# Performance work log

Measured on AMD Instinct MI355X. Metric: run time of the kernel, lower is better.

Reference implementation:

```python
import jax, jax.numpy as jnp
import numpy as np

N = 50000
HEADS1, HIM = 8, 16
NEG_SLOPE = 0.2


def gat_conv(x, src, dst, W, a_src, a_dst, bias, heads, out_dim, concat):
    n = x.shape[0]
    h = (x @ W).reshape(n, heads, out_dim)                      # [N,H,D]
    al_src = jnp.einsum('nhd,hd->nh', h, a_src)                  # [N,H]
    al_dst = jnp.einsum('nhd,hd->nh', h, a_dst)                  # [N,H]
    e = jax.nn.leaky_relu(al_src[src] + al_dst[dst], NEG_SLOPE)  # [E,H]
    # segment softmax over incoming edges of each destination node
    e_max = jax.ops.segment_max(e, dst, num_segments=n)
    e_max = jnp.where(jnp.isfinite(e_max), e_max, 0.0)
    ex = jnp.exp(e - e_max[dst])
    denom = jax.ops.segment_sum(ex, dst, num_segments=n)
    denom = jnp.where(denom == 0.0, 1.0, denom)
    alpha = ex / denom[dst]                                      # [E,H]
    msg = h[src] * alpha[:, :, None]                             # [E,H,D]
    out = jax.ops.segment_sum(msg, dst, num_segments=n)          # [N,H,D]
    out = out.reshape(n, heads * out_dim) if concat else out.mean(axis=1)
    return out + bias


def setup_inputs() -> dict:
    key = jax.random.key(0)
    ks = jax.random.split(key, 12)
    num_feature, out_feature, him = 128, 121, HIM
    E = 800000
    x = jax.random.normal(ks[0], (N, num_feature), dtype=jnp.float32)
    edge_index = jax.random.randint(ks[1], (2, E), 0, N, dtype=jnp.int64)
    s = 0.1
    W1 = jax.random.normal(ks[2], (num_feature, HEADS1 * him), dtype=jnp.float32) * s
    a_src1 = jax.random.normal(ks[3], (HEADS1, him), dtype=jnp.float32) * s
    a_dst1 = jax.random.normal(ks[4], (HEADS1, him), dtype=jnp.float32) * s
    b1 = jnp.zeros((HEADS1 * him,), dtype=jnp.float32)
    W2 = jax.random.normal(ks[5], (HEADS1 * him, out_feature), dtype=jnp.float32) * s
    a_src2 = jax.random.normal(ks[6], (1, out_feature), dtype=jnp.float32) * s
    a_dst2 = jax.random.normal(ks[7], (1, out_feature), dtype=jnp.float32) * s
    b2 = jnp.zeros((out_feature,), dtype=jnp.float32)
    return {"x": x, "edge_index": edge_index, "W1": W1, "a_src1": a_src1,
            "a_dst1": a_dst1, "b1": b1, "W2": W2, "a_src2": a_src2,
            "a_dst2": a_dst2, "b2": b2}


def reference(x, edge_index, W1, a_src1, a_dst1, b1, W2, a_src2, a_dst2, b2):
    n = x.shape[0]
    loops = jnp.arange(n, dtype=edge_index.dtype)
    src = jnp.concatenate([edge_index[0], loops])  # add self-loops (PyG default)
    dst = jnp.concatenate([edge_index[1], loops])
    h = gat_conv(x, src, dst, W1, a_src1, a_dst1, b1, HEADS1, HIM, True)
    h = jax.nn.relu(h)
    out = gat_conv(h, src, dst, W2, a_src2, a_dst2, b2, 1, W2.shape[1], True)
    return out
```

## Files before the change

### kernel.cpp

```cpp
#include <hip/hip_runtime.h>
#include <hip/hip_fp16.h>

#define NEG_SLOPE 0.2f

typedef __fp16 half8v __attribute__((ext_vector_type(8)));
typedef float f32x4 __attribute__((ext_vector_type(4)));

__device__ __forceinline__ float lrelu(float x) {
    return fmaxf(x, 0.0f) + NEG_SLOPE * fminf(x, 0.0f);
}

__device__ __forceinline__ unsigned fkey(float f) {
    unsigned u = __float_as_uint(f);
    return (u & 0x80000000u) ? ~u : (u | 0x80000000u);
}
__device__ __forceinline__ float funkey(unsigned k) {
    return __uint_as_float((k & 0x80000000u) ? (k & 0x7fffffffu) : ~k);
}


__global__ void pack_kernel(const int* __restrict__ src, const int* __restrict__ dst,
                            unsigned* __restrict__ kv, int E) {
    int e = blockIdx.x * 256 + threadIdx.x;
    if (e < E) kv[e] = ((unsigned)dst[e] << 16) | (unsigned)src[e];
}


__global__ __launch_bounds__(256) void scan_reduce(const int* __restrict__ cnt,
                                                   int* __restrict__ bsum, int n) {
    __shared__ int sm[256];
    int base = blockIdx.x * 1024 + threadIdx.x * 4;
    int s = 0;
#pragma unroll
    for (int j = 0; j < 4; ++j) {
        int i = base + j;
        if (i < n) s += cnt[i];
    }
    sm[threadIdx.x] = s;
    __syncthreads();
#pragma unroll
    for (int off = 128; off >= 1; off >>= 1) {
        if (threadIdx.x < off) sm[threadIdx.x] += sm[threadIdx.x + off];
        __syncthreads();
    }
    if (threadIdx.x == 0) bsum[blockIdx.x] = sm[0];
}

__global__ __launch_bounds__(64) void scan_bsum(int* __restrict__ bsum, int nb) {
    int v = (threadIdx.x < (unsigned)nb) ? bsum[threadIdx.x] : 0;
    int x = v;
#pragma unroll
    for (int off = 1; off < 64; off <<= 1) {
        int y = __shfl_up(x, off);
        if ((int)threadIdx.x >= off) x += y;
    }
    if (threadIdx.x < (unsigned)nb) bsum[threadIdx.x] = x - v;
}

__global__ __launch_bounds__(256) void scan_write(const int* __restrict__ cnt,
                                                  const int* __restrict__ bsum,
                                                  int* __restrict__ rp, int n) {
    __shared__ int sm[256];
    int base = blockIdx.x * 1024 + threadIdx.x * 4;
    int v[4];
    int s = 0;
#pragma unroll
    for (int j = 0; j < 4; ++j) {
        int i = base + j;
        v[j] = (i < n) ? cnt[i] : 0;
        s += v[j];
    }
    sm[threadIdx.x] = s;
    __syncthreads();
#pragma unroll
    for (int off = 1; off < 256; off <<= 1) {
        int y = (threadIdx.x >= off) ? sm[threadIdx.x - off] : 0;
        __syncthreads();
        sm[threadIdx.x] += y;
        __syncthreads();
    }
    int run = sm[threadIdx.x] - s + bsum[blockIdx.x];
#pragma unroll
    for (int j = 0; j < 4; ++j) {
        int i = base + j;
        if (i < n) {
            rp[i] = run;
            run += v[j];
            if (i == n - 1) rp[n] = run;
        }
    }
}


template <int SH>
__global__ __launch_bounds__(256) void rhist_kernel(const unsigned* __restrict__ kv,
                                                    int* __restrict__ h, int E, int nblk) {
    __shared__ int lh[256];
    lh[threadIdx.x] = 0;
    __syncthreads();
    int base = blockIdx.x * 4096;
#pragma unroll
    for (int j = 0; j < 16; ++j) {
        int i = base + j * 256 + threadIdx.x;
        if (i < E) atomicAdd(&lh[(kv[i] >> SH) & 255], 1);
    }
    __syncthreads();
    h[threadIdx.x * nblk + blockIdx.x] = lh[threadIdx.x];
}


template <int SH>
__global__ __launch_bounds__(256) void rscat_kernel(const unsigned* __restrict__ in,
                                                    unsigned* __restrict__ outv,
                                                    const int* __restrict__ scanned,
                                                    int E, int nblk) {
    __shared__ unsigned items[4096];
    __shared__ unsigned sorted[4096];
    __shared__ int lh[256], lstart[256], rbase[256];
    __shared__ int wcnt[4][256];

    int tid = threadIdx.x, blk = blockIdx.x;
    int base = blk * 4096;
    int k = min(4096, E - base);
    lh[tid] = 0;
    rbase[tid] = 0;
#pragma unroll
    for (int j = 0; j < 16; ++j) {
        int idx = j * 256 + tid;
        items[idx] = (base + idx < E) ? in[base + idx] : 0u;
    }
    __syncthreads();
#pragma unroll
    for (int j = 0; j < 16; ++j) {
        int idx = j * 256 + tid;
        if (idx < k) atomicAdd(&lh[(items[idx] >> SH) & 255], 1);
    }
    __syncthreads();
    int sv = lh[tid];
    lstart[tid] = sv;
    __syncthreads();
    for (int off = 1; off < 256; off <<= 1) {
        int y = (tid >= off) ? lstart[tid - off] : 0;
        __syncthreads();
        lstart[tid] += y;
        __syncthreads();
    }
    int excl = lstart[tid] - sv;
    __syncthreads();
    lstart[tid] = excl;
    __syncthreads();

    int lane = tid & 63, wave = tid >> 6;
    for (int it = 0; it < 16; ++it) {
        int idx = it * 256 + tid;
        unsigned v = items[idx];
        int d = (v >> SH) & 255;
        bool valid = idx < k;
        unsigned long long vm = __ballot(valid);
        unsigned long long m = vm;
#pragma unroll
        for (int b = 0; b < 8; ++b) {
            unsigned long long bb = __ballot((d >> b) & 1);
            m &= ((d >> b) & 1) ? bb : ~bb;
        }
        int lanerank = __popcll(m & ((1ull << lane) - 1ull));
        int wtot = __popcll(m);
        wcnt[0][tid] = 0; wcnt[1][tid] = 0; wcnt[2][tid] = 0; wcnt[3][tid] = 0;
        __syncthreads();
        if (valid && lanerank == 0) wcnt[wave][d] = wtot;
        __syncthreads();
        if (valid) {
            int cw = 0;
            for (int w = 0; w < wave; ++w) cw += wcnt[w][d];
            sorted[lstart[d] + rbase[d] + cw + lanerank] = v;
        }
        __syncthreads();
        rbase[tid] += wcnt[0][tid] + wcnt[1][tid] + wcnt[2][tid] + wcnt[3][tid];
        __syncthreads();
    }
#pragma unroll
    for (int j = 0; j < 16; ++j) {
        int i = j * 256 + tid;
        if (i < k) {
            unsigned v = sorted[i];
            int d = (v >> SH) & 255;
            outv[scanned[d * nblk + blk] + (i - lstart[d])] = v;
        }
    }
}


__global__ void rp_kernel(const unsigned* __restrict__ kv, int* __restrict__ rp,
                          int E, int N) {
    int i = blockIdx.x * 256 + threadIdx.x;
    if (i >= E) return;
    int cur = (int)(kv[i] >> 16);
    int prev = (i == 0) ? -1 : (int)(kv[i - 1] >> 16);
    for (int t = prev + 1; t <= cur; ++t) rp[t] = i;
    if (i == E - 1)
        for (int t = cur + 1; t <= N; ++t) rp[t] = E;
}


template <int H>
__global__ __launch_bounds__(256) void gmax_kernel(const float* __restrict__ a,
                                                   unsigned* __restrict__ gm, int total) {
    __shared__ unsigned sm[256];
    unsigned loc = 0;
    int stride = 256 * gridDim.x;
    for (int i = blockIdx.x * 256 + threadIdx.x; i < total; i += stride)
        loc = max(loc, fkey(a[i]));
    sm[threadIdx.x] = loc;
    __syncthreads();
    for (int off = 128; off >= H; off >>= 1) {
        if (threadIdx.x < off) sm[threadIdx.x] = max(sm[threadIdx.x], sm[threadIdx.x + off]);
        __syncthreads();
    }
    if (threadIdx.x < H) atomicMax(&gm[threadIdx.x], sm[threadIdx.x]);
}


__global__ __launch_bounds__(256) void cvt_half_kernel(const float* __restrict__ in,
                                                       __half* __restrict__ out, int total8) {
    int i = blockIdx.x * 256 + threadIdx.x;
    if (i >= total8) return;
    const float4* ip = (const float4*)in + (size_t)i * 2;
    float4 a = ip[0], b = ip[1];
    union { float4 f4; __half2 h[4]; } u;
    u.h[0] = __floats2half2_rn(a.x, a.y);
    u.h[1] = __floats2half2_rn(a.z, a.w);
    u.h[2] = __floats2half2_rn(b.x, b.y);
    u.h[3] = __floats2half2_rn(b.z, b.w);
    *((float4*)out + i) = u.f4;
}


template <int NC>
__global__ __launch_bounds__(256) void gemm_mfma(const __half* __restrict__ A,
                                                 const float* __restrict__ B,
                                                 __half* __restrict__ C, int M) {
    __shared__ __half Bt[128][136];

    {
        int t = threadIdx.x;
        int c = t & 127;
        int kq = t >> 7;
#pragma unroll
        for (int ch = 0; ch < 8; ++ch) {
            int k0 = kq * 64 + ch * 8;
            half8v hv;
#pragma unroll
            for (int j = 0; j < 8; ++j) {
                float v = (c < NC) ? B[(size_t)(k0 + j) * NC + c] : 0.0f;
                hv[j] = (__fp16)v;
            }
            *(half8v*)&Bt[c][k0] = hv;
        }
    }
    __syncthreads();

    const int wid = threadIdx.x >> 6;
    const int lane = threadIdx.x & 63;
    const int li = lane & 15;
    const int lg = lane >> 4;

    int row = blockIdx.x * 64 + wid * 16 + li;
    int rowc = min(row, M - 1);
    const half8v* Ap = (const half8v*)(A + (size_t)rowc * 128);

    half8v a[4];
#pragma unroll
    for (int ks = 0; ks < 4; ++ks) a[ks] = Ap[ks * 4 + lg];

    f32x4 acc[8];
#pragma unroll
    for (int ct = 0; ct < 8; ++ct) acc[ct] = (f32x4)0.0f;

#pragma unroll
    for (int ks = 0; ks < 4; ++ks) {
#pragma unroll
        for (int ct = 0; ct < 8; ++ct) {
            half8v b = *(const half8v*)&Bt[ct * 16 + li][ks * 32 + 8 * lg];
            acc[ct] = __builtin_amdgcn_mfma_f32_16x16x32_f16(a[ks], b, acc[ct], 0, 0, 0);
        }
    }

    int orow = blockIdx.x * 64 + wid * 16 + 4 * lg;
#pragma unroll
    for (int ct = 0; ct < 8; ++ct) {
#pragma unroll
        for (int r = 0; r < 4; ++r) {
            int rr = orow + r;
            if (rr < M) C[(size_t)rr * 128 + ct * 16 + li] = __float2half(acc[ct][r]);
        }
    }
}


__global__ void al1_kernel(const __half* __restrict__ h1h, const float* __restrict__ as,
                           const float* __restrict__ ad, float* __restrict__ alS,
                           float* __restrict__ alD, int N) {
    int g = blockIdx.x * 256 + threadIdx.x;
    if (g >= N * 8) return;
    int r = g >> 3, h = g & 7;
    const __half2* hp = (const __half2*)(h1h + (size_t)r * 128 + h * 16);
    const float* sp = as + h * 16;
    const float* dp = ad + h * 16;
    float s = 0.f, d = 0.f;
#pragma unroll
    for (int q = 0; q < 8; ++q) {
        float2 v = __half22float2(hp[q]);
        s = fmaf(v.x, sp[2 * q], s);
        d = fmaf(v.x, dp[2 * q], d);
        s = fmaf(v.y, sp[2 * q + 1], s);
        d = fmaf(v.y, dp[2 * q + 1], d);
    }
    alS[g] = s;
    alD[g] = d;
}

__global__ __launch_bounds__(256) void al2_kernel(const __half* __restrict__ h3h,
                                                  const float* __restrict__ as,
                                                  const float* __restrict__ ad,
                                                  float* __restrict__ alS,
                                                  float* __restrict__ alD, int N, int NC) {
    int lane = threadIdx.x & 63;
    int r = blockIdx.x * 4 + (threadIdx.x >> 6);
    if (r >= N) return;
    float s = 0.f, d = 0.f;
    for (int c = lane; c < NC; c += 64) {
        float v = __half2float(h3h[(size_t)r * 128 + c]);
        s = fmaf(v, as[c], s);
        d = fmaf(v, ad[c], d);
    }
#pragma unroll
    for (int off = 32; off; off >>= 1) {
        s += __shfl_down(s, off);
        d += __shfl_down(d, off);
    }
    if (lane == 0) { alS[r] = s; alD[r] = d; }
}


__global__ __launch_bounds__(256) void agg1_kernel(
    const __half* __restrict__ h1h, const float* __restrict__ alS,
    const float* __restrict__ alD, const float* __restrict__ b1,
    const int* __restrict__ rp, const unsigned* __restrict__ kv,
    const unsigned* __restrict__ gm, __half* __restrict__ h2h, int N) {
    int t = blockIdx.x * 4 + (threadIdx.x >> 6);
    if (t >= N) return;
    int lane = threadIdx.x & 63;
    int h = lane >> 3;

    float adh = alD[t * 8 + h];
    float mh = lrelu(funkey(gm[h]) + adh);
    int e0 = rp[t], e1 = rp[t + 1];

    float ex = __expf(lrelu(alS[t * 8 + h] + adh) - mh);
    float dsum = ex;
    float2 hs = __half22float2(*(const __half2*)(h1h + (size_t)t * 128 + 2 * lane));
    float fx = ex * hs.x, fy = ex * hs.y;

    int e = e0;
    for (; e + 4 <= e1; e += 4) {
        int s0 = (int)(kv[e] & 0xFFFFu), s1 = (int)(kv[e + 1] & 0xFFFFu);
        int s2 = (int)(kv[e + 2] & 0xFFFFu), s3 = (int)(kv[e + 3] & 0xFFFFu);
        float w0 = __expf(lrelu(alS[s0 * 8 + h] + adh) - mh);
        float w1 = __expf(lrelu(alS[s1 * 8 + h] + adh) - mh);
        float w2 = __expf(lrelu(alS[s2 * 8 + h] + adh) - mh);
        float w3 = __expf(lrelu(alS[s3 * 8 + h] + adh) - mh);
        float2 f0 = __half22float2(*(const __half2*)(h1h + (size_t)s0 * 128 + 2 * lane));
        float2 f1 = __half22float2(*(const __half2*)(h1h + (size_t)s1 * 128 + 2 * lane));
        float2 f2 = __half22float2(*(const __half2*)(h1h + (size_t)s2 * 128 + 2 * lane));
        float2 f3 = __half22float2(*(const __half2*)(h1h + (size_t)s3 * 128 + 2 * lane));
        dsum += (w0 + w1) + (w2 + w3);
        fx = fmaf(w0, f0.x, fx); fy = fmaf(w0, f0.y, fy);
        fx = fmaf(w1, f1.x, fx); fy = fmaf(w1, f1.y, fy);
        fx = fmaf(w2, f2.x, fx); fy = fmaf(w2, f2.y, fy);
        fx = fmaf(w3, f3.x, fx); fy = fmaf(w3, f3.y, fy);
    }
    for (; e < e1; ++e) {
        int s0 = (int)(kv[e] & 0xFFFFu);
        float w0 = __expf(lrelu(alS[s0 * 8 + h] + adh) - mh);
        float2 f0 = __half22float2(*(const __half2*)(h1h + (size_t)s0 * 128 + 2 * lane));
        dsum += w0;
        fx = fmaf(w0, f0.x, fx); fy = fmaf(w0, f0.y, fy);
    }
    float inv = 1.0f / dsum;
    float2 bb = *(const float2*)(b1 + 2 * lane);
    float ox = fmaxf(fmaf(fx, inv, bb.x), 0.0f);
    float oy = fmaxf(fmaf(fy, inv, bb.y), 0.0f);
    *(__half2*)(h2h + (size_t)t * 128 + 2 * lane) = __floats2half2_rn(ox, oy);
}


__global__ __launch_bounds__(256) void agg2_kernel(
    const __half* __restrict__ h3h, const float* __restrict__ alS,
    const float* __restrict__ alD, const float* __restrict__ b2,
    const int* __restrict__ rp, const unsigned* __restrict__ kv,
    const unsigned* __restrict__ gm, float* __restrict__ out, int N, int NC) {
    int t = blockIdx.x * 4 + (threadIdx.x >> 6);
    if (t >= N) return;
    int lane = threadIdx.x & 63;

    float adT = alD[t];
    float m = lrelu(funkey(gm[0]) + adT);
    int e0 = rp[t], e1 = rp[t + 1];

    float ex = __expf(lrelu(alS[t] + adT) - m);
    float dsum = ex;
    float2 hs = __half22float2(*(const __half2*)(h3h + (size_t)t * 128 + 2 * lane));
    float fx = ex * hs.x, fy = ex * hs.y;

    int e = e0;
    for (; e + 4 <= e1; e += 4) {
        int s0 = (int)(kv[e] & 0xFFFFu), s1 = (int)(kv[e + 1] & 0xFFFFu);
        int s2 = (int)(kv[e + 2] & 0xFFFFu), s3 = (int)(kv[e + 3] & 0xFFFFu);
        float w0 = __expf(lrelu(alS[s0] + adT) - m);
        float w1 = __expf(lrelu(alS[s1] + adT) - m);
        float w2 = __expf(lrelu(alS[s2] + adT) - m);
        float w3 = __expf(lrelu(alS[s3] + adT) - m);
        float2 f0 = __half22float2(*(const __half2*)(h3h + (size_t)s0 * 128 + 2 * lane));
        float2 f1 = __half22float2(*(const __half2*)(h3h + (size_t)s1 * 128 + 2 * lane));
        float2 f2 = __half22float2(*(const __half2*)(h3h + (size_t)s2 * 128 + 2 * lane));
        float2 f3 = __half22float2(*(const __half2*)(h3h + (size_t)s3 * 128 + 2 * lane));
        dsum += (w0 + w1) + (w2 + w3);
        fx = fmaf(w0, f0.x, fx); fy = fmaf(w0, f0.y, fy);
        fx = fmaf(w1, f1.x, fx); fy = fmaf(w1, f1.y, fy);
        fx = fmaf(w2, f2.x, fx); fy = fmaf(w2, f2.y, fy);
        fx = fmaf(w3, f3.x, fx); fy = fmaf(w3, f3.y, fy);
    }
    for (; e < e1; ++e) {
        int s0 = (int)(kv[e] & 0xFFFFu);
        float w0 = __expf(lrelu(alS[s0] + adT) - m);
        float2 f0 = __half22float2(*(const __half2*)(h3h + (size_t)s0 * 128 + 2 * lane));
        dsum += w0;
        fx = fmaf(w0, f0.x, fx); fy = fmaf(w0, f0.y, fy);
    }
    float inv = 1.0f / dsum;
    int c0 = 2 * lane, c1 = 2 * lane + 1;
    if (c0 < NC) out[(size_t)t * NC + c0] = fmaf(fx, inv, b2[c0]);
    if (c1 < NC) out[(size_t)t * NC + c1] = fmaf(fy, inv, b2[c1]);
}


extern "C" void kernel_launch(void* const* d_in, const int* in_sizes, int n_in,
                              void* d_out, int out_size, void* d_ws, size_t ws_size,
                              hipStream_t stream) {
    const float* x   = (const float*)d_in[0];
    const int*   ei  = (const int*)d_in[1];
    const float* W1  = (const float*)d_in[2];
    const float* aS1 = (const float*)d_in[3];
    const float* aD1 = (const float*)d_in[4];
    const float* b1  = (const float*)d_in[5];
    const float* W2  = (const float*)d_in[6];
    const float* aS2 = (const float*)d_in[7];
    const float* aD2 = (const float*)d_in[8];
    const float* b2  = (const float*)d_in[9];
    float* out = (float*)d_out;

    const int N = in_sizes[0] / 128;
    const int E = in_sizes[1] / 2;
    const int NC2 = 121;

    const int NBLK = (E + 4095) / 4096;
    const int HN = 256 * NBLK;

    size_t off = 0;
    auto alloc = [&](size_t bytes) {
        size_t o = off;
        off = (off + bytes + 255) & ~(size_t)255;
        return o;
    };
    char* ws = (char*)d_ws;
    unsigned* kv0  = (unsigned*)(ws + alloc((size_t)E * 4));
    unsigned* kv1  = (unsigned*)(ws + alloc((size_t)E * 4));
    int*      h    = (int*)(ws + alloc((size_t)(HN + 1) * 4));
    int*      hs   = (int*)(ws + alloc((size_t)(HN + 1) * 4));
    int*      rp   = (int*)(ws + alloc((size_t)(N + 1) * 4));
    int*      bsum = (int*)(ws + alloc(64 * 4));
    float*    alS1 = (float*)(ws + alloc((size_t)N * 8 * 4));
    float*    alD1 = (float*)(ws + alloc((size_t)N * 8 * 4));
    float*    alS2 = (float*)(ws + alloc((size_t)N * 4));
    float*    alD2 = (float*)(ws + alloc((size_t)N * 4));
    unsigned* gm1  = (unsigned*)(ws + alloc(8 * 4));
    unsigned* gm2  = (unsigned*)(ws + alloc(4));
    __half*   xh   = (__half*)(ws + alloc((size_t)N * 128 * 2));
    __half*   h1h  = (__half*)(ws + alloc((size_t)N * 128 * 2));
    __half*   h2h  = (__half*)(ws + alloc((size_t)N * 128 * 2));
    __half*   h3h  = h1h;
    if (ws_size < off) return;

    const int* src = ei;
    const int* dst = ei + E;

    hipMemsetAsync(gm1, 0, 8 * 4, stream);
    hipMemsetAsync(gm2, 0, 4, stream);

    int eb = (E + 255) / 256;
    int snb = (HN + 1023) / 1024;

    pack_kernel<<<eb, 256, 0, stream>>>(src, dst, kv0, E);
    rhist_kernel<16><<<NBLK, 256, 0, stream>>>(kv0, h, E, NBLK);
    scan_reduce<<<snb, 256, 0, stream>>>(h, bsum, HN);
    scan_bsum<<<1, 64, 0, stream>>>(bsum, snb);
    scan_write<<<snb, 256, 0, stream>>>(h, bsum, hs, HN);
    rscat_kernel<16><<<NBLK, 256, 0, stream>>>(kv0, kv1, hs, E, NBLK);
    rhist_kernel<24><<<NBLK, 256, 0, stream>>>(kv1, h, E, NBLK);
    scan_reduce<<<snb, 256, 0, stream>>>(h, bsum, HN);
    scan_bsum<<<1, 64, 0, stream>>>(bsum, snb);
    scan_write<<<snb, 256, 0, stream>>>(h, bsum, hs, HN);
    rscat_kernel<24><<<NBLK, 256, 0, stream>>>(kv1, kv0, hs, E, NBLK);
    rp_kernel<<<eb, 256, 0, stream>>>(kv0, rp, E, N);

    int cvb = (N * 128 / 8 + 255) / 256;
    cvt_half_kernel<<<cvb, 256, 0, stream>>>(x, xh, N * 128 / 8);

    int gmb = (N + 63) / 64;
    int ab = (N + 3) / 4;
    gemm_mfma<128><<<gmb, 256, 0, stream>>>(xh, W1, h1h, N);
    al1_kernel<<<(N * 8 + 255) / 256, 256, 0, stream>>>(h1h, aS1, aD1, alS1, alD1, N);
    gmax_kernel<8><<<128, 256, 0, stream>>>(alS1, gm1, N * 8);
    agg1_kernel<<<ab, 256, 0, stream>>>(h1h, alS1, alD1, b1, rp, kv0, gm1, h2h, N);

    gemm_mfma<121><<<gmb, 256, 0, stream>>>(h2h, W2, h3h, N);
    al2_kernel<<<ab, 256, 0, stream>>>(h3h, aS2, aD2, alS2, alD2, N, NC2);
    gmax_kernel<1><<<128, 256, 0, stream>>>(alS2, gm2, N);
    agg2_kernel<<<ab, 256, 0, stream>>>(h3h, alS2, alD2, b2, rp, kv0, gm2, out, N, NC2);
}
```

Measured before the change: 237.3 us.

## Precompute per-edge attention weights and fuse fp32-to-half conversion into GEMM

Drops the separate x-to-half conversion kernel; the first GEMM now loads fp32 rows and converts them in registers. Per-edge exponentiated attention weights are computed in new edge-parallel kernels (stored as half for layer 1, float for layer 2). The aggregation kernels then read these weights sequentially instead of gathering alS per source and recomputing exp, and each splits the denominator sum into two accumulators. The cost is two extra launches and extra traffic to write and reread the edge-weight arrays, and layer 1 weights lose precision by being stored in half.

```diff
diff --git a/kernel.cpp b/kernel.cpp
--- a/kernel.cpp
+++ b/kernel.cpp
@@ -156,8 +156,7 @@
         unsigned v = items[idx];
         int d = (v >> SH) & 255;
         bool valid = idx < k;
-        unsigned long long vm = __ballot(valid);
-        unsigned long long m = vm;
+        unsigned long long m = __ballot(valid);
 #pragma unroll
         for (int b = 0; b < 8; ++b) {
             unsigned long long bb = __ballot((d >> b) & 1);
@@ -220,23 +219,34 @@
 }
 
 
-__global__ __launch_bounds__(256) void cvt_half_kernel(const float* __restrict__ in,
-                                                       __half* __restrict__ out, int total8) {
-    int i = blockIdx.x * 256 + threadIdx.x;
-    if (i >= total8) return;
-    const float4* ip = (const float4*)in + (size_t)i * 2;
-    float4 a = ip[0], b = ip[1];
-    union { float4 f4; __half2 h[4]; } u;
-    u.h[0] = __floats2half2_rn(a.x, a.y);
-    u.h[1] = __floats2half2_rn(a.z, a.w);
-    u.h[2] = __floats2half2_rn(b.x, b.y);
-    u.h[3] = __floats2half2_rn(b.z, b.w);
-    *((float4*)out + i) = u.f4;
-}
-
-
-template <int NC>
-__global__ __launch_bounds__(256) void gemm_mfma(const __half* __restrict__ A,
+__global__ void w1_kernel(const unsigned* __restrict__ kv, const float* __restrict__ alS,
+                          const float* __restrict__ alD, const unsigned* __restrict__ gm,
+                          __half* __restrict__ w1v, int E8) {
+    int g = blockIdx.x * 256 + threadIdx.x;
+    if (g >= E8) return;
+    int e = g >> 3, h = g & 7;
+    unsigned k = kv[e];
+    int s = (int)(k & 0xFFFFu), t = (int)(k >> 16);
+    float adT = alD[t * 8 + h];
+    float m = lrelu(funkey(gm[h]) + adT);
+    w1v[g] = __float2half(__expf(lrelu(alS[s * 8 + h] + adT) - m));
+}
+
+
+__global__ void w2_kernel(const unsigned* __restrict__ kv, const float* __restrict__ alS,
+                          const float* __restrict__ alD, const unsigned* __restrict__ gm,
+                          float* __restrict__ w2v, int E) {
+    int e = blockIdx.x * 256 + threadIdx.x;
+    if (e >= E) return;
+    unsigned k = kv[e];
+    int s = (int)(k & 0xFFFFu), t = (int)(k >> 16);
+    float adT = alD[t];
+    w2v[e] = __expf(lrelu(alS[s] + adT) - lrelu(funkey(gm[0]) + adT));
+}
+
+
+template <int NC, typename AT>
+__global__ __launch_bounds__(256) void gemm_mfma(const AT* __restrict__ A,
                                                  const float* __restrict__ B,
                                                  __half* __restrict__ C, int M) {
     __shared__ __half Bt[128][136];
@@ -266,11 +276,22 @@
 
     int row = blockIdx.x * 64 + wid * 16 + li;
     int rowc = min(row, M - 1);
-    const half8v* Ap = (const half8v*)(A + (size_t)rowc * 128);
 
     half8v a[4];
 #pragma unroll
-    for (int ks = 0; ks < 4; ++ks) a[ks] = Ap[ks * 4 + lg];
+    for (int ks = 0; ks < 4; ++ks) {
+        int q = ks * 4 + lg;
+        if constexpr (sizeof(AT) == 2) {
+            a[ks] = *((const half8v*)(A + (size_t)rowc * 128) + q);
+        } else {
+            const float4* p = (const float4*)(A + (size_t)rowc * 128) + 2 * q;
+            float4 a0 = p[0], a1 = p[1];
+            half8v hv;
+            hv[0] = (__fp16)a0.x; hv[1] = (__fp16)a0.y; hv[2] = (__fp16)a0.z; hv[3] = (__fp16)a0.w;
+            hv[4] = (__fp16)a1.x; hv[5] = (__fp16)a1.y; hv[6] = (__fp16)a1.z; hv[7] = (__fp16)a1.w;
+            a[ks] = hv;
+        }
+    }
 
     f32x4 acc[8];
 #pragma unroll
@@ -346,7 +367,8 @@
     const __half* __restrict__ h1h, const float* __restrict__ alS,
     const float* __restrict__ alD, const float* __restrict__ b1,
     const int* __restrict__ rp, const unsigned* __restrict__ kv,
-    const unsigned* __restrict__ gm, __half* __restrict__ h2h, int N) {
+    const __half* __restrict__ w1v, const unsigned* __restrict__ gm,
+    __half* __restrict__ h2h, int N) {
     int t = blockIdx.x * 4 + (threadIdx.x >> 6);
     if (t >= N) return;
     int lane = threadIdx.x & 63;
@@ -357,7 +379,7 @@
     int e0 = rp[t], e1 = rp[t + 1];
 
     float ex = __expf(lrelu(alS[t * 8 + h] + adh) - mh);
-    float dsum = ex;
+    float dsum = ex, dsum2 = 0.f;
     float2 hs = __half22float2(*(const __half2*)(h1h + (size_t)t * 128 + 2 * lane));
     float fx = ex * hs.x, fy = ex * hs.y;
 
@@ -365,15 +387,16 @@
     for (; e + 4 <= e1; e += 4) {
         int s0 = (int)(kv[e] & 0xFFFFu), s1 = (int)(kv[e + 1] & 0xFFFFu);
         int s2 = (int)(kv[e + 2] & 0xFFFFu), s3 = (int)(kv[e + 3] & 0xFFFFu);
-        float w0 = __expf(lrelu(alS[s0 * 8 + h] + adh) - mh);
-        float w1 = __expf(lrelu(alS[s1 * 8 + h] + adh) - mh);
-        float w2 = __expf(lrelu(alS[s2 * 8 + h] + adh) - mh);
-        float w3 = __expf(lrelu(alS[s3 * 8 + h] + adh) - mh);
+        float w0 = __half2float(w1v[(size_t)(e + 0) * 8 + h]);
+        float w1 = __half2float(w1v[(size_t)(e + 1) * 8 + h]);
+        float w2 = __half2float(w1v[(size_t)(e + 2) * 8 + h]);
+        float w3 = __half2float(w1v[(size_t)(e + 3) * 8 + h]);
         float2 f0 = __half22float2(*(const __half2*)(h1h + (size_t)s0 * 128 + 2 * lane));
         float2 f1 = __half22float2(*(const __half2*)(h1h + (size_t)s1 * 128 + 2 * lane));
         float2 f2 = __half22float2(*(const __half2*)(h1h + (size_t)s2 * 128 + 2 * lane));
         float2 f3 = __half22float2(*(const __half2*)(h1h + (size_t)s3 * 128 + 2 * lane));
-        dsum += (w0 + w1) + (w2 + w3);
+        dsum += w0 + w1;
+        dsum2 += w2 + w3;
         fx = fmaf(w0, f0.x, fx); fy = fmaf(w0, f0.y, fy);
         fx = fmaf(w1, f1.x, fx); fy = fmaf(w1, f1.y, fy);
         fx = fmaf(w2, f2.x, fx); fy = fmaf(w2, f2.y, fy);
@@ -381,11 +404,12 @@
     }
     for (; e < e1; ++e) {
         int s0 = (int)(kv[e] & 0xFFFFu);
-        float w0 = __expf(lrelu(alS[s0 * 8 + h] + adh) - mh);
+        float w0 = __half2float(w1v[(size_t)e * 8 + h]);
         float2 f0 = __half22float2(*(const __half2*)(h1h + (size_t)s0 * 128 + 2 * lane));
         dsum += w0;
         fx = fmaf(w0, f0.x, fx); fy = fmaf(w0, f0.y, fy);
     }
+    dsum += dsum2;
     float inv = 1.0f / dsum;
     float2 bb = *(const float2*)(b1 + 2 * lane);
     float ox = fmaxf(fmaf(fx, inv, bb.x), 0.0f);
@@ -398,7 +422,8 @@
     const __half* __restrict__ h3h, const float* __restrict__ alS,
     const float* __restrict__ alD, const float* __restrict__ b2,
     const int* __restrict__ rp, const unsigned* __restrict__ kv,
-    const unsigned* __restrict__ gm, float* __restrict__ out, int N, int NC) {
+    const float* __restrict__ w2v, const unsigned* __restrict__ gm,
+    float* __restrict__ out, int N, int NC) {
     int t = blockIdx.x * 4 + (threadIdx.x >> 6);
     if (t >= N) return;
     int lane = threadIdx.x & 63;
@@ -408,7 +433,7 @@
     int e0 = rp[t], e1 = rp[t + 1];
 
     float ex = __expf(lrelu(alS[t] + adT) - m);
-    float dsum = ex;
+    float dsum = ex, dsum2 = 0.f;
     float2 hs = __half22float2(*(const __half2*)(h3h + (size_t)t * 128 + 2 * lane));
     float fx = ex * hs.x, fy = ex * hs.y;
 
@@ -416,15 +441,13 @@
     for (; e + 4 <= e1; e += 4) {
         int s0 = (int)(kv[e] & 0xFFFFu), s1 = (int)(kv[e + 1] & 0xFFFFu);
         int s2 = (int)(kv[e + 2] & 0xFFFFu), s3 = (int)(kv[e + 3] & 0xFFFFu);
-        float w0 = __expf(lrelu(alS[s0] + adT) - m);
-        float w1 = __expf(lrelu(alS[s1] + adT) - m);
-        float w2 = __expf(lrelu(alS[s2] + adT) - m);
-        float w3 = __expf(lrelu(alS[s3] + adT) - m);
+        float w0 = w2v[e], w1 = w2v[e + 1], w2 = w2v[e + 2], w3 = w2v[e + 3];
         float2 f0 = __half22float2(*(const __half2*)(h3h + (size_t)s0 * 128 + 2 * lane));
         float2 f1 = __half22float2(*(const __half2*)(h3h + (size_t)s1 * 128 + 2 * lane));
         float2 f2 = __half22float2(*(const __half2*)(h3h + (size_t)s2 * 128 + 2 * lane));
         float2 f3 = __half22float2(*(const __half2*)(h3h + (size_t)s3 * 128 + 2 * lane));
-        dsum += (w0 + w1) + (w2 + w3);
+        dsum += w0 + w1;
+        dsum2 += w2 + w3;
         fx = fmaf(w0, f0.x, fx); fy = fmaf(w0, f0.y, fy);
         fx = fmaf(w1, f1.x, fx); fy = fmaf(w1, f1.y, fy);
         fx = fmaf(w2, f2.x, fx); fy = fmaf(w2, f2.y, fy);
@@ -432,11 +455,12 @@
     }
     for (; e < e1; ++e) {
         int s0 = (int)(kv[e] & 0xFFFFu);
-        float w0 = __expf(lrelu(alS[s0] + adT) - m);
+        float w0 = w2v[e];
         float2 f0 = __half22float2(*(const __half2*)(h3h + (size_t)s0 * 128 + 2 * lane));
         dsum += w0;
         fx = fmaf(w0, f0.x, fx); fy = fmaf(w0, f0.y, fy);
     }
+    dsum += dsum2;
     float inv = 1.0f / dsum;
     int c0 = 2 * lane, c1 = 2 * lane + 1;
     if (c0 < NC) out[(size_t)t * NC + c0] = fmaf(fx, inv, b2[c0]);
@@ -485,10 +509,11 @@
     float*    alD2 = (float*)(ws + alloc((size_t)N * 4));
     unsigned* gm1  = (unsigned*)(ws + alloc(8 * 4));
     unsigned* gm2  = (unsigned*)(ws + alloc(4));
-    __half*   xh   = (__half*)(ws + alloc((size_t)N * 128 * 2));
+    __half*   w1v  = (__half*)(ws + alloc((size_t)E * 8 * 2));
     __half*   h1h  = (__half*)(ws + alloc((size_t)N * 128 * 2));
     __half*   h2h  = (__half*)(ws + alloc((size_t)N * 128 * 2));
     __half*   h3h  = h1h;
+    float*    w2v  = (float*)kv1;
     if (ws_size < off) return;
 
     const int* src = ei;
@@ -513,18 +538,17 @@
     rscat_kernel<24><<<NBLK, 256, 0, stream>>>(kv1, kv0, hs, E, NBLK);
     rp_kernel<<<eb, 256, 0, stream>>>(kv0, rp, E, N);
 
-    int cvb = (N * 128 / 8 + 255) / 256;
-    cvt_half_kernel<<<cvb, 256, 0, stream>>>(x, xh, N * 128 / 8);
-
     int gmb = (N + 63) / 64;
     int ab = (N + 3) / 4;
-    gemm_mfma<128><<<gmb, 256, 0, stream>>>(xh, W1, h1h, N);
+    gemm_mfma<128, float><<<gmb, 256, 0, stream>>>(x, W1, h1h, N);
     al1_kernel<<<(N * 8 + 255) / 256, 256, 0, stream>>>(h1h, aS1, aD1, alS1, alD1, N);
     gmax_kernel<8><<<128, 256, 0, stream>>>(alS1, gm1, N * 8);
-    agg1_kernel<<<ab, 256, 0, stream>>>(h1h, alS1, alD1, b1, rp, kv0, gm1, h2h, N);
-
-    gemm_mfma<121><<<gmb, 256, 0, stream>>>(h2h, W2, h3h, N);
+    w1_kernel<<<(E * 8 + 255) / 256, 256, 0, stream>>>(kv0, alS1, alD1, gm1, w1v, E * 8);
+    agg1_kernel<<<ab, 256, 0, stream>>>(h1h, alS1, alD1, b1, rp, kv0, w1v, gm1, h2h, N);
+
+    gemm_mfma<121, __half><<<gmb, 256, 0, stream>>>(h2h, W2, h3h, N);
     al2_kernel<<<ab, 256, 0, stream>>>(h3h, aS2, aD2, alS2, alD2, N, NC2);
     gmax_kernel<1><<<128, 256, 0, stream>>>(alS2, gm2, N);
-    agg2_kernel<<<ab, 256, 0, stream>>>(h3h, alS2, alD2, b2, rp, kv0, gm2, out, N, NC2);
-}
+    w2_kernel<<<eb, 256, 0, stream>>>(kv0, alS2, alD2, gm2, w2v, E);
+    agg2_kernel<<<ab, 256, 0, stream>>>(h3h, alS2, alD2, b2, rp, kv0, w2v, gm2, out, N, NC2);
+}
```

Result: slower. 249.9 us (+5.3%).
